# Kernel tuning notes

Hardware: AMD Instinct MI355X
Metric: run time of the kernel (lower is better)

The kernel has to match this reference:

```python
import jax, jax.numpy as jnp
import numpy as np
import math

KEY_SIZE = 128  # init arg; scale = 1/sqrt(key_size)


def setup_inputs() -> dict:
    key = jax.random.key(0)
    kq, kk, kv = jax.random.split(key, 3)
    B, LQ, LK, D, DV = 16, 2048, 2048, 128, 128
    q = jax.random.normal(kq, (B, LQ, D), dtype=jnp.float32)
    k = jax.random.normal(kk, (B, LK, D), dtype=jnp.float32)
    v = jax.random.normal(kv, (B, LK, DV), dtype=jnp.float32)
    return {"q": q, "k": k, "v": v}


def reference(q, k, v):
    scale = 1.0 / math.sqrt(KEY_SIZE)
    # scores: [B, Lq, Lk]
    scores = jnp.einsum('bqd,bkd->bqk', q, k) * scale
    probs = jax.nn.softmax(scores, axis=-1)
    # dropout with p=0.0 is identity (eval-equivalent)
    return jnp.einsum('bqk,bkv->bqv', probs, v)
```

## Files before the change

kernel.cpp:

```cpp
#include <hip/hip_runtime.h>
#include <hip/hip_bf16.h>

typedef float f32x4 __attribute__((ext_vector_type(4)));
typedef short bf16x8 __attribute__((ext_vector_type(8)));

constexpr int NB = 16, LQ = 2048, LK = 2048, D = 128, DV = 128;
constexpr int QBLK = 64, KVBLK = 64, NT = LK / KVBLK;
constexpr float SCALE = 0.08838834764831843f;
constexpr float LOG2E = 1.4426950408889634f;
constexpr float QSCALE = SCALE * LOG2E;

__device__ __forceinline__ unsigned short f2bfs(float f) {
  __hip_bfloat16 h = __float2bfloat16(f);
  return __builtin_bit_cast(unsigned short, h);
}

__device__ __forceinline__ unsigned short f2bf(float f) {
  unsigned int u = __float_as_uint(f);
  u += 0x7FFFu + ((u >> 16) & 1u);
  return (unsigned short)(u >> 16);
}

__device__ __forceinline__ int swz2(int row) {
  return (row ^ (row >> 1) ^ (row >> 3)) & 7;
}

typedef const __attribute__((address_space(1))) void* gas1_t;
typedef __attribute__((address_space(3))) void* las3_t;
__device__ __forceinline__ void gload16(const void* g, void* l) {
  __builtin_amdgcn_global_load_lds((gas1_t)g, (las3_t)l, 16, 0, 0);
}

__global__ __launch_bounds__(256) void conv_bf16(const float* __restrict__ in,
                                                 unsigned short* __restrict__ out,
                                                 float scale) {
  int i = blockIdx.x * 256 + threadIdx.x;
  f32x4 a = ((const f32x4*)in)[2 * i];
  f32x4 b = ((const f32x4*)in)[2 * i + 1];
  bf16x8 r;
  #pragma unroll
  for (int j = 0; j < 4; ++j) {
    r[j]     = (short)f2bfs(a[j] * scale);
    r[4 + j] = (short)f2bfs(b[j] * scale);
  }
  ((bf16x8*)out)[i] = r;
}

__global__ __launch_bounds__(256) void conv_vt(const float* __restrict__ v,
                                               unsigned short* __restrict__ vt) {
  __shared__ __align__(16) unsigned short tb[64 * 64];
  const int tid = threadIdx.x;
  const int k0 = blockIdx.x * 64, dv0 = blockIdx.y * 64, b = blockIdx.z;
  {
    const int kk = tid >> 2, dd0 = (tid & 3) * 16;
    const float* src = v + ((long)(b * LK + k0 + kk)) * DV + dv0 + dd0;
    f32x4 a0 = ((const f32x4*)src)[0];
    f32x4 a1 = ((const f32x4*)src)[1];
    f32x4 a2 = ((const f32x4*)src)[2];
    f32x4 a3 = ((const f32x4*)src)[3];
    bf16x8 r0, r1;
    #pragma unroll
    for (int j = 0; j < 4; ++j) {
      r0[j] = (short)f2bfs(a0[j]); r0[4 + j] = (short)f2bfs(a1[j]);
      r1[j] = (short)f2bfs(a2[j]); r1[4 + j] = (short)f2bfs(a3[j]);
    }
    int ch = dd0 >> 3;
    *(bf16x8*)&tb[kk * 64 + ((ch ^ swz2(kk)) << 3)] = r0;
    *(bf16x8*)&tb[kk * 64 + (((ch + 1) ^ swz2(kk)) << 3)] = r1;
  }
  __syncthreads();
  {
    const int dv = tid >> 2, ks = (tid & 3) * 16;
    bf16x8 w0, w1;
    #pragma unroll
    for (int j = 0; j < 8; ++j) {
      int r0 = ks + j, r1 = ks + 8 + j;
      w0[j] = (short)tb[r0 * 64 + (((dv >> 3) ^ swz2(r0)) << 3) + (dv & 7)];
      w1[j] = (short)tb[r1 * 64 + (((dv >> 3) ^ swz2(r1)) << 3) + (dv & 7)];
    }
    unsigned short* dst = vt + ((long)(b * DV + dv0 + dv)) * LK + k0 + ks;
    *(bf16x8*)dst = w0;
    *(bf16x8*)(dst + 8) = w1;
  }
}

__global__ __launch_bounds__(256, 2) void attn_fwd2(
    const float* __restrict__ qp, const unsigned short* __restrict__ wsK,
    const unsigned short* __restrict__ wsVt, float* __restrict__ op) {
  __shared__ __align__(16) unsigned short sm[32768];

  const int tid = threadIdx.x;
  const int wid = tid >> 6;
  const int lane = tid & 63;
  const int g = lane >> 4;
  const int c = lane & 15;

  const int bid = blockIdx.x;
  const int sbid = (bid & 7) * 64 + (bid >> 3);
  const int b = sbid >> 5;
  const int qb = (sbid & 31) * QBLK;

  const float* qrow = qp + ((long)(b * LQ + qb + wid * 16 + c)) * D;
  bf16x8 aq[4];
  #pragma unroll
  for (int ks = 0; ks < 4; ++ks) {
    f32x4 x0 = *(const f32x4*)(qrow + ks * 32 + g * 8);
    f32x4 x1 = *(const f32x4*)(qrow + ks * 32 + g * 8 + 4);
    #pragma unroll
    for (int j = 0; j < 4; ++j) {
      aq[ks][j]     = (short)f2bfs(x0[j] * QSCALE);
      aq[ks][4 + j] = (short)f2bfs(x1[j] * QSCALE);
    }
  }

  const unsigned short* kbatch = wsK + (long)b * LK * D;
  const unsigned short* vbatch = wsVt + (long)b * DV * LK;

  auto stage = [&](int buf, int kv0) {
    const unsigned short* ksrc = kbatch + (long)kv0 * D;
    #pragma unroll
    for (int it = 0; it < 4; ++it) {
      int ci = it * 256 + tid, row = ci >> 4, c16 = ci & 15;
      gload16(ksrc + row * D + ((c16 ^ swz2(row)) << 3), &sm[buf * 16384 + ci * 8]);
    }
    #pragma unroll
    for (int it = 0; it < 4; ++it) {
      int ci = it * 256 + tid, row = ci >> 3, c8 = ci & 7;
      gload16(vbatch + (long)row * LK + kv0 + ((c8 ^ swz2(row)) << 3),
              &sm[buf * 16384 + 8192 + ci * 8]);
    }
  };

  stage(0, 0);
  __syncthreads();

  f32x4 o[8];
  f32x4 fz = {0.f, 0.f, 0.f, 0.f};
  #pragma unroll
  for (int i = 0; i < 8; ++i) o[i] = fz;
  float m_s = -1e30f, l_s = 0.f;

  for (int t = 0; t < NT; ++t) {
    const int cur = t & 1;
    if (t + 1 < NT) stage(cur ^ 1, (t + 1) * KVBLK);
    const int kb = cur * 16384, vb = kb + 8192;

    f32x4 s[4];
    #pragma unroll
    for (int i = 0; i < 4; ++i) s[i] = fz;
    __builtin_amdgcn_s_setprio(1);
    #pragma unroll
    for (int tt = 0; tt < 4; ++tt) {
      int row = 32 * (tt >> 1) + 4 * (tt & 1) + (c & 3) + ((c >> 2) << 3);
      int sz = swz2(row);
      #pragma unroll
      for (int ks = 0; ks < 4; ++ks) {
        bf16x8 ak = *(const bf16x8*)&sm[kb + row * 128 + ((((ks << 2) + g) ^ sz) << 3)];
        s[tt] = __builtin_amdgcn_mfma_f32_16x16x32_bf16(ak, aq[ks], s[tt], 0, 0, 0);
      }
    }
    __builtin_amdgcn_s_setprio(0);

    float pm = s[0][0];
    #pragma unroll
    for (int tt = 0; tt < 4; ++tt)
      #pragma unroll
      for (int r = 0; r < 4; ++r) pm = fmaxf(pm, s[tt][r]);
    pm = fmaxf(pm, __shfl_xor(pm, 16));
    pm = fmaxf(pm, __shfl_xor(pm, 32));
    if (!__all(pm <= m_s + 8.0f)) {
      float mn = fmaxf(m_s, pm);
      float al = exp2f(m_s - mn);
      l_s *= al;
      float al4[4];
      #pragma unroll
      for (int r = 0; r < 4; ++r) al4[r] = __shfl(al, 4 * g + r);
      #pragma unroll
      for (int dvt = 0; dvt < 8; ++dvt)
        #pragma unroll
        for (int r = 0; r < 4; ++r) o[dvt][r] *= al4[r];
      m_s = mn;
    }
    float sum = 0.f;
    #pragma unroll
    for (int tt = 0; tt < 4; ++tt)
      #pragma unroll
      for (int r = 0; r < 4; ++r) {
        float p = exp2f(s[tt][r] - m_s);
        s[tt][r] = p;
        sum += p;
      }
    sum += __shfl_xor(sum, 16);
    sum += __shfl_xor(sum, 32);
    l_s += sum;

    bf16x8 pa[2];
    #pragma unroll
    for (int ks = 0; ks < 2; ++ks) {
      #pragma unroll
      for (int j = 0; j < 4; ++j) {
        pa[ks][j]     = (short)f2bfs(s[2 * ks][j]);
        pa[ks][4 + j] = (short)f2bfs(s[2 * ks + 1][j]);
      }
    }

    __builtin_amdgcn_s_setprio(1);
    #pragma unroll
    for (int ks = 0; ks < 2; ++ks) {
      #pragma unroll
      for (int dvt = 0; dvt < 8; ++dvt) {
        int row = dvt * 16 + c;
        bf16x8 vbf = *(const bf16x8*)&sm[vb + row * 64 + ((((ks << 2) + g) ^ swz2(row)) << 3)];
        o[dvt] = __builtin_amdgcn_mfma_f32_16x16x32_bf16(pa[ks], vbf, o[dvt], 0, 0, 0);
      }
    }
    __builtin_amdgcn_s_setprio(0);

    __syncthreads();
  }

  float linv[4];
  #pragma unroll
  for (int r = 0; r < 4; ++r) linv[r] = 1.f / __shfl(l_s, 4 * g + r);
  float* dst = op + ((long)(b * LQ + qb + wid * 16)) * DV;
  #pragma unroll
  for (int r = 0; r < 4; ++r)
    #pragma unroll
    for (int dvt = 0; dvt < 8; ++dvt)
      dst[(4 * g + r) * DV + dvt * 16 + c] = o[dvt][r] * linv[r];
}

__device__ __forceinline__ int swzc(int row, int c16) {
  return c16 ^ ((row ^ (row >> 3)) & 7);
}

__global__ __launch_bounds__(256, 2) void attn_fwd(
    const float* __restrict__ qp, const float* __restrict__ kp,
    const float* __restrict__ vp, float* __restrict__ op) {
  __shared__ __align__(16) unsigned short smm[28672];
  const int tid = threadIdx.x, wid = tid >> 6, lane = tid & 63;
  const int g = lane >> 4, c = lane & 15;
  const int b = blockIdx.y, qb = blockIdx.x * QBLK;
  const float* qg = qp + ((long)b * LQ + qb) * D;
  const float* kg = kp + (long)b * LK * D;
  const float* vg = vp + (long)b * LK * DV;
  #pragma unroll
  for (int it = 0; it < 4; ++it) {
    int ch = it * 256 + tid, row = ch >> 4, c16 = ch & 15;
    const float* src = qg + row * D + c16 * 8;
    f32x4 f0 = *(const f32x4*)(src);
    f32x4 f1 = *(const f32x4*)(src + 4);
    bf16x8 fr;
    #pragma unroll
    for (int j = 0; j < 4; ++j) {
      fr[j] = (short)f2bf(f0[j] * SCALE);
      fr[4 + j] = (short)f2bf(f1[j] * SCALE);
    }
    *(bf16x8*)&smm[row * 128 + swzc(row, c16) * 8] = fr;
  }
  __syncthreads();
  bf16x8 aq[4];
  #pragma unroll
  for (int ks = 0; ks < 4; ++ks) {
    int row = wid * 16 + c;
    aq[ks] = *(const bf16x8*)&smm[row * 128 + swzc(row, ks * 4 + g) * 8];
  }
  f32x4 o[8]; f32x4 fz = {0.f, 0.f, 0.f, 0.f};
  #pragma unroll
  for (int i = 0; i < 8; ++i) o[i] = fz;
  float m_r[4] = {-1e30f, -1e30f, -1e30f, -1e30f};
  float l_r[4] = {0.f, 0.f, 0.f, 0.f};
  const int pbase = 24576 + wid * 1024;
  for (int kv0 = 0; kv0 < LK; kv0 += KVBLK) {
    __syncthreads();
    const float* ksrc = kg + (long)kv0 * D;
    #pragma unroll
    for (int it = 0; it < 4; ++it) {
      int ch = it * 256 + tid, row = ch >> 4, c16 = ch & 15;
      const float* src = ksrc + row * D + c16 * 8;
      f32x4 f0 = *(const f32x4*)(src);
      f32x4 f1 = *(const f32x4*)(src + 4);
      bf16x8 fr;
      #pragma unroll
      for (int j = 0; j < 4; ++j) { fr[j] = (short)f2bf(f0[j]); fr[4 + j] = (short)f2bf(f1[j]); }
      *(bf16x8*)&smm[8192 + row * 128 + swzc(row, c16) * 8] = fr;
    }
    {
      const float* vsrc = vg + (long)kv0 * DV;
      int dvq = (tid & 31) * 4, kg8 = tid >> 5;
      f32x4 col[8];
      #pragma unroll
      for (int j = 0; j < 8; ++j) col[j] = *(const f32x4*)(vsrc + (kg8 * 8 + j) * DV + dvq);
      #pragma unroll
      for (int i = 0; i < 4; ++i) {
        int dv = dvq + i;
        bf16x8 fr;
        #pragma unroll
        for (int j = 0; j < 8; ++j) fr[j] = (short)f2bf(col[j][i]);
        *(bf16x8*)&smm[16384 + dv * 64 + swzc(dv, kg8) * 8] = fr;
      }
    }
    __syncthreads();
    f32x4 s[4];
    #pragma unroll
    for (int i = 0; i < 4; ++i) s[i] = fz;
    #pragma unroll
    for (int ks = 0; ks < 4; ++ks) {
      #pragma unroll
      for (int t = 0; t < 4; ++t) {
        int row = t * 16 + c;
        bf16x8 bk = *(const bf16x8*)&smm[8192 + row * 128 + swzc(row, ks * 4 + g) * 8];
        s[t] = __builtin_amdgcn_mfma_f32_16x16x32_bf16(aq[ks], bk, s[t], 0, 0, 0);
      }
    }
    #pragma unroll
    for (int r = 0; r < 4; ++r) {
      float pm = fmaxf(fmaxf(s[0][r], s[1][r]), fmaxf(s[2][r], s[3][r]));
      pm = fmaxf(pm, __shfl_xor(pm, 1));
      pm = fmaxf(pm, __shfl_xor(pm, 2));
      pm = fmaxf(pm, __shfl_xor(pm, 4));
      pm = fmaxf(pm, __shfl_xor(pm, 8));
      float mn = fmaxf(m_r[r], pm);
      float al = exp2f((m_r[r] - mn) * LOG2E);
      float sum = 0.f;
      #pragma unroll
      for (int t = 0; t < 4; ++t) {
        float p = exp2f((s[t][r] - mn) * LOG2E);
        s[t][r] = p; sum += p;
      }
      sum += __shfl_xor(sum, 1); sum += __shfl_xor(sum, 2);
      sum += __shfl_xor(sum, 4); sum += __shfl_xor(sum, 8);
      l_r[r] = l_r[r] * al + sum; m_r[r] = mn;
      #pragma unroll
      for (int dvt = 0; dvt < 8; ++dvt) o[dvt][r] *= al;
    }
    #pragma unroll
    for (int t = 0; t < 4; ++t)
      #pragma unroll
      for (int r = 0; r < 4; ++r) {
        int row = g * 4 + r, colx = c + 16 * t;
        smm[pbase + row * 64 + swzc(row, colx >> 3) * 8 + (colx & 7)] = f2bf(s[t][r]);
      }
    #pragma unroll
    for (int ks = 0; ks < 2; ++ks) {
      bf16x8 pa = *(const bf16x8*)&smm[pbase + c * 64 + swzc(c, ks * 4 + g) * 8];
      #pragma unroll
      for (int dvt = 0; dvt < 8; ++dvt) {
        int row = dvt * 16 + c;
        bf16x8 vb2 = *(const bf16x8*)&smm[16384 + row * 64 + swzc(row, ks * 4 + g) * 8];
        o[dvt] = __builtin_amdgcn_mfma_f32_16x16x32_bf16(pa, vb2, o[dvt], 0, 0, 0);
      }
    }
  }
  float* dst = op + ((long)b * LQ + qb + wid * 16) * DV;
  #pragma unroll
  for (int r = 0; r < 4; ++r) {
    float inv = 1.f / l_r[r];
    #pragma unroll
    for (int dvt = 0; dvt < 8; ++dvt)
      dst[(g * 4 + r) * DV + dvt * 16 + c] = o[dvt][r] * inv;
  }
}

extern "C" void kernel_launch(void* const* d_in, const int* in_sizes, int n_in,
                              void* d_out, int out_size, void* d_ws, size_t ws_size,
                              hipStream_t stream) {
  const float* q = (const float*)d_in[0];
  const float* k = (const float*)d_in[1];
  const float* v = (const float*)d_in[2];
  float* out = (float*)d_out;

  const size_t kelems = (size_t)NB * LK * D;
  const size_t need = kelems * 2 * 2;
  if (ws_size >= need) {
    unsigned short* wsK = (unsigned short*)d_ws;
    unsigned short* wsVt = wsK + kelems;
    conv_bf16<<<dim3((int)(kelems / 8 / 256)), dim3(256), 0, stream>>>(k, wsK, 1.0f);
    conv_vt<<<dim3(LK / 64, DV / 64, NB), dim3(256), 0, stream>>>(v, wsVt);
    attn_fwd2<<<dim3(NB * LQ / QBLK), dim3(256), 0, stream>>>(q, wsK, wsVt, out);
  } else {
    attn_fwd<<<dim3(LQ / QBLK, NB), dim3(256), 0, stream>>>(q, k, v, out);
  }
}
```

Baseline: 80.65 us.

## Rewrite attention kernel with 32x32 MFMA, split-KV waves and deeper prefetch

Replaces the 256-thread attention kernel with a 512-thread version. Each block handles 128 query rows, and each wave owns 32 rows. Two wave groups each process half the KV sequence and their results are merged through LDS at the end. Scores and PV now use 32x32x16 bf16 MFMA, which removes cross-lane shuffles for the row max and sum. Loads are prefetched two tiles ahead with explicit vmcnt waits and raw barriers. The costs are more LDS (128KB), higher register pressure from f32x16 accumulators, and an extra combine step.

```diff
diff --git a/kernel.cpp b/kernel.cpp
--- a/kernel.cpp
+++ b/kernel.cpp
@@ -2,10 +2,13 @@
 #include <hip/hip_bf16.h>
 
 typedef float f32x4 __attribute__((ext_vector_type(4)));
+typedef float f32x16 __attribute__((ext_vector_type(16)));
 typedef short bf16x8 __attribute__((ext_vector_type(8)));
+typedef unsigned u32x4 __attribute__((ext_vector_type(4)));
 
 constexpr int NB = 16, LQ = 2048, LK = 2048, D = 128, DV = 128;
-constexpr int QBLK = 64, KVBLK = 64, NT = LK / KVBLK;
+constexpr int KVBLK = 64;
+constexpr int NTH = 16;
 constexpr float SCALE = 0.08838834764831843f;
 constexpr float LOG2E = 1.4426950408889634f;
 constexpr float QSCALE = SCALE * LOG2E;
@@ -25,10 +28,26 @@
   return (row ^ (row >> 1) ^ (row >> 3)) & 7;
 }
 
+__device__ __forceinline__ int swap23(int m) {
+  return (m & ~12) | ((m & 4) << 1) | ((m & 8) >> 1);
+}
+
 typedef const __attribute__((address_space(1))) void* gas1_t;
 typedef __attribute__((address_space(3))) void* las3_t;
 __device__ __forceinline__ void gload16(const void* g, void* l) {
   __builtin_amdgcn_global_load_lds((gas1_t)g, (las3_t)l, 16, 0, 0);
+}
+
+__device__ __forceinline__ unsigned pk2(float lo, float hi) {
+  unsigned short a = f2bfs(lo), b = f2bfs(hi);
+  return (unsigned)a | ((unsigned)b << 16);
+}
+
+__device__ __forceinline__ void mk_pb(const f32x16& s, bf16x8& pe, bf16x8& po) {
+  u32x4 e = {pk2(s[0], s[1]), pk2(s[2], s[3]), pk2(s[4], s[5]), pk2(s[6], s[7])};
+  pe = __builtin_bit_cast(bf16x8, e);
+  u32x4 od = {pk2(s[8], s[9]), pk2(s[10], s[11]), pk2(s[12], s[13]), pk2(s[14], s[15])};
+  po = __builtin_bit_cast(bf16x8, od);
 }
 
 __global__ __launch_bounds__(256) void conv_bf16(const float* __restrict__ in,
@@ -84,150 +103,188 @@
   }
 }
 
-__global__ __launch_bounds__(256, 2) void attn_fwd2(
+__global__ __launch_bounds__(512, 2) void attn_fwd5(
     const float* __restrict__ qp, const unsigned short* __restrict__ wsK,
     const unsigned short* __restrict__ wsVt, float* __restrict__ op) {
-  __shared__ __align__(16) unsigned short sm[32768];
+  __shared__ __align__(16) unsigned short sm[65536];
 
   const int tid = threadIdx.x;
   const int wid = tid >> 6;
+  const int h2  = wid >> 2;
   const int lane = tid & 63;
-  const int g = lane >> 4;
-  const int c = lane & 15;
+  const int q32 = lane & 31;
+  const int hi  = lane >> 5;
+  const int ht  = tid & 255;
 
   const int bid = blockIdx.x;
-  const int sbid = (bid & 7) * 64 + (bid >> 3);
-  const int b = sbid >> 5;
-  const int qb = (sbid & 31) * QBLK;
-
-  const float* qrow = qp + ((long)(b * LQ + qb + wid * 16 + c)) * D;
-  bf16x8 aq[4];
-  #pragma unroll
-  for (int ks = 0; ks < 4; ++ks) {
-    f32x4 x0 = *(const f32x4*)(qrow + ks * 32 + g * 8);
-    f32x4 x1 = *(const f32x4*)(qrow + ks * 32 + g * 8 + 4);
-    #pragma unroll
-    for (int j = 0; j < 4; ++j) {
-      aq[ks][j]     = (short)f2bfs(x0[j] * QSCALE);
-      aq[ks][4 + j] = (short)f2bfs(x1[j] * QSCALE);
-    }
-  }
+  const int sbid = (bid & 7) * 32 + (bid >> 3);
+  const int b = sbid >> 4;
+  const int qb = (sbid & 15) * 128;
+  const int qwave = qb + (wid & 3) * 32;
+
+  bf16x8 aq[8];
+  {
+    const float* qrow = qp + ((long)(b * LQ + qwave + q32)) * D + hi * 8;
+    #pragma unroll
+    for (int st = 0; st < 8; ++st) {
+      f32x4 x0 = *(const f32x4*)(qrow + st * 16);
+      f32x4 x1 = *(const f32x4*)(qrow + st * 16 + 4);
+      #pragma unroll
+      for (int j = 0; j < 4; ++j) {
+        aq[st][j]     = (short)f2bfs(x0[j] * QSCALE);
+        aq[st][4 + j] = (short)f2bfs(x1[j] * QSCALE);
+      }
+    }
+  }
+  __builtin_amdgcn_sched_barrier(0);
 
   const unsigned short* kbatch = wsK + (long)b * LK * D;
   const unsigned short* vbatch = wsVt + (long)b * DV * LK;
-
-  auto stage = [&](int buf, int kv0) {
-    const unsigned short* ksrc = kbatch + (long)kv0 * D;
-    #pragma unroll
-    for (int it = 0; it < 4; ++it) {
-      int ci = it * 256 + tid, row = ci >> 4, c16 = ci & 15;
-      gload16(ksrc + row * D + ((c16 ^ swz2(row)) << 3), &sm[buf * 16384 + ci * 8]);
-    }
-    #pragma unroll
-    for (int it = 0; it < 4; ++it) {
-      int ci = it * 256 + tid, row = ci >> 3, c8 = ci & 7;
-      gload16(vbatch + (long)row * LK + kv0 + ((c8 ^ swz2(row)) << 3),
-              &sm[buf * 16384 + 8192 + ci * 8]);
-    }
+  const int kvbase = h2 * 1024;
+  const int lbase = h2 * 32768;
+
+  const unsigned short* ksp[4];
+  const unsigned short* vsp[4];
+  unsigned ldk[4], ldv[4];
+  #pragma unroll
+  for (int it = 0; it < 4; ++it) {
+    int ci = it * 256 + ht;
+    int krow = ci >> 4, kc16 = ci & 15;
+    ksp[it] = kbatch + (long)kvbase * D + swap23(krow) * D +
+              ((kc16 ^ swz2(krow)) << 3);
+    ldk[it] = lbase + ci * 8;
+    int vrow = ci >> 3, vc8 = ci & 7;
+    vsp[it] = vbatch + (long)vrow * LK + kvbase + ((vc8 ^ swz2(vrow)) << 3);
+    ldv[it] = lbase + 8192 + ci * 8;
+  }
+
+  auto stage = [&](int buf, int t) {
+    const int ko = t * (KVBLK * D);
+    const int vo = t * KVBLK;
+    const int lb = buf * 16384;
+    #pragma unroll
+    for (int it = 0; it < 4; ++it)
+      gload16(ksp[it] + ko, &sm[ldk[it] + lb]);
+    #pragma unroll
+    for (int it = 0; it < 4; ++it)
+      gload16(vsp[it] + vo, &sm[ldv[it] + lb]);
   };
 
   stage(0, 0);
-  __syncthreads();
-
-  f32x4 o[8];
-  f32x4 fz = {0.f, 0.f, 0.f, 0.f};
-  #pragma unroll
-  for (int i = 0; i < 8; ++i) o[i] = fz;
+  stage(1, 1);
+
+  f32x16 o[4];
+  #pragma unroll
+  for (int mt = 0; mt < 4; ++mt) o[mt] = (f32x16){};
   float m_s = -1e30f, l_s = 0.f;
 
-  for (int t = 0; t < NT; ++t) {
+  for (int t = 0; t < NTH; ++t) {
+    if (t < NTH - 1) {
+      asm volatile("s_waitcnt vmcnt(8)" ::: "memory");
+    } else {
+      asm volatile("s_waitcnt vmcnt(0)" ::: "memory");
+    }
+    __builtin_amdgcn_sched_barrier(0);
+    __builtin_amdgcn_s_barrier();
+    __builtin_amdgcn_sched_barrier(0);
+
     const int cur = t & 1;
-    if (t + 1 < NT) stage(cur ^ 1, (t + 1) * KVBLK);
-    const int kb = cur * 16384, vb = kb + 8192;
-
-    f32x4 s[4];
-    #pragma unroll
-    for (int i = 0; i < 4; ++i) s[i] = fz;
+    const int kb = lbase + cur * 16384, vb = kb + 8192;
+
+    f32x16 s0 = (f32x16){}, s1 = (f32x16){};
     __builtin_amdgcn_s_setprio(1);
     #pragma unroll
-    for (int tt = 0; tt < 4; ++tt) {
-      int row = 32 * (tt >> 1) + 4 * (tt & 1) + (c & 3) + ((c >> 2) << 3);
-      int sz = swz2(row);
-      #pragma unroll
-      for (int ks = 0; ks < 4; ++ks) {
-        bf16x8 ak = *(const bf16x8*)&sm[kb + row * 128 + ((((ks << 2) + g) ^ sz) << 3)];
-        s[tt] = __builtin_amdgcn_mfma_f32_16x16x32_bf16(ak, aq[ks], s[tt], 0, 0, 0);
-      }
+    for (int st = 0; st < 8; ++st) {
+      const int c16 = 2 * st + hi;
+      const int r0 = q32;
+      bf16x8 k0 = *(const bf16x8*)&sm[kb + r0 * 128 + ((c16 ^ swz2(r0)) << 3)];
+      s0 = __builtin_amdgcn_mfma_f32_32x32x16_bf16(k0, aq[st], s0, 0, 0, 0);
+      const int r1 = 32 + q32;
+      bf16x8 k1 = *(const bf16x8*)&sm[kb + r1 * 128 + ((c16 ^ swz2(r1)) << 3)];
+      s1 = __builtin_amdgcn_mfma_f32_32x32x16_bf16(k1, aq[st], s1, 0, 0, 0);
     }
     __builtin_amdgcn_s_setprio(0);
 
-    float pm = s[0][0];
-    #pragma unroll
-    for (int tt = 0; tt < 4; ++tt)
-      #pragma unroll
-      for (int r = 0; r < 4; ++r) pm = fmaxf(pm, s[tt][r]);
-    pm = fmaxf(pm, __shfl_xor(pm, 16));
+    float pm = s0[0];
+    #pragma unroll
+    for (int i = 1; i < 16; ++i) pm = fmaxf(pm, s0[i]);
+    #pragma unroll
+    for (int i = 0; i < 16; ++i) pm = fmaxf(pm, s1[i]);
     pm = fmaxf(pm, __shfl_xor(pm, 32));
     if (!__all(pm <= m_s + 8.0f)) {
       float mn = fmaxf(m_s, pm);
       float al = exp2f(m_s - mn);
       l_s *= al;
-      float al4[4];
-      #pragma unroll
-      for (int r = 0; r < 4; ++r) al4[r] = __shfl(al, 4 * g + r);
-      #pragma unroll
-      for (int dvt = 0; dvt < 8; ++dvt)
+      #pragma unroll
+      for (int mt = 0; mt < 4; ++mt)
         #pragma unroll
-        for (int r = 0; r < 4; ++r) o[dvt][r] *= al4[r];
+        for (int i = 0; i < 16; ++i) o[mt][i] *= al;
       m_s = mn;
     }
     float sum = 0.f;
     #pragma unroll
-    for (int tt = 0; tt < 4; ++tt)
-      #pragma unroll
-      for (int r = 0; r < 4; ++r) {
-        float p = exp2f(s[tt][r] - m_s);
-        s[tt][r] = p;
-        sum += p;
-      }
-    sum += __shfl_xor(sum, 16);
-    sum += __shfl_xor(sum, 32);
-    l_s += sum;
-
-    bf16x8 pa[2];
-    #pragma unroll
-    for (int ks = 0; ks < 2; ++ks) {
-      #pragma unroll
-      for (int j = 0; j < 4; ++j) {
-        pa[ks][j]     = (short)f2bfs(s[2 * ks][j]);
-        pa[ks][4 + j] = (short)f2bfs(s[2 * ks + 1][j]);
-      }
-    }
+    for (int i = 0; i < 16; ++i) { s0[i] = exp2f(s0[i] - m_s); sum += s0[i]; }
+    #pragma unroll
+    for (int i = 0; i < 16; ++i) { s1[i] = exp2f(s1[i] - m_s); sum += s1[i]; }
+    l_s += sum + __shfl_xor(sum, 32);
+
+    bf16x8 pb[4];
+    mk_pb(s0, pb[0], pb[1]);
+    mk_pb(s1, pb[2], pb[3]);
 
     __builtin_amdgcn_s_setprio(1);
     #pragma unroll
-    for (int ks = 0; ks < 2; ++ks) {
-      #pragma unroll
-      for (int dvt = 0; dvt < 8; ++dvt) {
-        int row = dvt * 16 + c;
-        bf16x8 vbf = *(const bf16x8*)&sm[vb + row * 64 + ((((ks << 2) + g) ^ swz2(row)) << 3)];
-        o[dvt] = __builtin_amdgcn_mfma_f32_16x16x32_bf16(pa[ks], vbf, o[dvt], 0, 0, 0);
+    for (int ks = 0; ks < 4; ++ks) {
+      const int c8 = 2 * ks + hi;
+      #pragma unroll
+      for (int mt = 0; mt < 4; ++mt) {
+        const int row = mt * 32 + q32;
+        bf16x8 vf = *(const bf16x8*)&sm[vb + row * 64 + ((c8 ^ swz2(row)) << 3)];
+        o[mt] = __builtin_amdgcn_mfma_f32_32x32x16_bf16(vf, pb[ks], o[mt], 0, 0, 0);
       }
     }
     __builtin_amdgcn_s_setprio(0);
 
-    __syncthreads();
-  }
-
-  float linv[4];
-  #pragma unroll
-  for (int r = 0; r < 4; ++r) linv[r] = 1.f / __shfl(l_s, 4 * g + r);
-  float* dst = op + ((long)(b * LQ + qb + wid * 16)) * DV;
-  #pragma unroll
-  for (int r = 0; r < 4; ++r)
-    #pragma unroll
-    for (int dvt = 0; dvt < 8; ++dvt)
-      dst[(4 * g + r) * DV + dvt * 16 + c] = o[dvt][r] * linv[r];
+    __builtin_amdgcn_sched_barrier(0);
+    __builtin_amdgcn_s_barrier();
+    __builtin_amdgcn_sched_barrier(0);
+
+    if (t < NTH - 2) stage(cur, t + 2);
+  }
+
+  float* scr = (float*)sm;
+  float* wreg = scr + (size_t)(wid & 3) * 4352;
+  __syncthreads();
+  if (h2 == 1) {
+    #pragma unroll
+    for (int j4 = 0; j4 < 16; ++j4) {
+      const int mt = j4 >> 2, a = j4 & 3;
+      f32x4 v = {o[mt][4 * a], o[mt][4 * a + 1], o[mt][4 * a + 2], o[mt][4 * a + 3]};
+      *(f32x4*)&wreg[lane * 64 + ((j4 ^ (lane & 15)) << 2)] = v;
+    }
+    wreg[4096 + lane * 2] = m_s;
+    wreg[4096 + lane * 2 + 1] = l_s;
+  }
+  __syncthreads();
+  if (h2 == 0) {
+    const float m1 = wreg[4096 + lane * 2];
+    const float l1 = wreg[4096 + lane * 2 + 1];
+    const float mm = fmaxf(m_s, m1);
+    float a0 = exp2f(m_s - mm), a1 = exp2f(m1 - mm);
+    const float inv = 1.f / (a0 * l_s + a1 * l1);
+    a0 *= inv;
+    a1 *= inv;
+    float* dst = op + ((long)(b * LQ + qwave + q32)) * DV;
+    #pragma unroll
+    for (int j4 = 0; j4 < 16; ++j4) {
+      const int mt = j4 >> 2, a = j4 & 3;
+      f32x4 pv = *(const f32x4*)&wreg[lane * 64 + ((j4 ^ (lane & 15)) << 2)];
+      f32x4 r;
+      #pragma unroll
+      for (int i = 0; i < 4; ++i) r[i] = a0 * o[mt][4 * a + i] + a1 * pv[i];
+      *(f32x4*)&dst[32 * mt + 8 * a + 4 * hi] = r;
+    }
+  }
 }
 
 __device__ __forceinline__ int swzc(int row, int c16) {
@@ -240,7 +297,7 @@
   __shared__ __align__(16) unsigned short smm[28672];
   const int tid = threadIdx.x, wid = tid >> 6, lane = tid & 63;
   const int g = lane >> 4, c = lane & 15;
-  const int b = blockIdx.y, qb = blockIdx.x * QBLK;
+  const int b = blockIdx.y, qb = blockIdx.x * 64;
   const float* qg = qp + ((long)b * LQ + qb) * D;
   const float* kg = kp + (long)b * LK * D;
   const float* vg = vp + (long)b * LK * DV;
@@ -377,8 +434,8 @@
     unsigned short* wsVt = wsK + kelems;
     conv_bf16<<<dim3((int)(kelems / 8 / 256)), dim3(256), 0, stream>>>(k, wsK, 1.0f);
     conv_vt<<<dim3(LK / 64, DV / 64, NB), dim3(256), 0, stream>>>(v, wsVt);
-    attn_fwd2<<<dim3(NB * LQ / QBLK), dim3(256), 0, stream>>>(q, wsK, wsVt, out);
+    attn_fwd5<<<dim3(NB * LQ / 128), dim3(512), 0, stream>>>(q, wsK, wsVt, out);
   } else {
-    attn_fwd<<<dim3(LQ / QBLK, NB), dim3(256), 0, stream>>>(q, k, v, out);
-  }
-}
+    attn_fwd<<<dim3(LQ / 64, NB), dim3(256), 0, stream>>>(q, k, v, out);
+  }
+}
```

New measurement: 75.55 us. 6.3% less time.
